# Kernel optimization log

Measured on AMD Instinct MI355X. Metric: run time of the kernel, lower is better.

The kernel has to match this reference:

```python
import jax, jax.numpy as jnp
import numpy as np

L = 32   # latent_dim == enc_dim
ND = 1   # node feature dim (single node type)
B, N = 8, 256
M = 3 * L           # message / Encoder output dim = 2*latent + enc = 96
DIN = 2 * (ND + L) + L  # Encoder input dim = 2*node + 2*latent + enc = 98


def _glorot(key, shape):
    fan_in, fan_out = shape
    s = jnp.sqrt(6.0 / (fan_in + fan_out))
    return jax.random.uniform(key, shape, jnp.float32, -s, s)


def setup_inputs() -> dict:
    key = jax.random.key(0)
    ks = jax.random.split(key, 14)
    return {
        "xs": jax.random.normal(ks[0], (B, N, ND), jnp.float32),
        "hs": jax.random.normal(ks[1], (B, N, L), jnp.float32),
        "e_feat": jax.random.normal(ks[2], (B, N, N, 1), jnp.float32),
        "adj": jax.random.randint(ks[3], (B, N, N), 0, 2, jnp.int32),
        "W_e": _glorot(ks[4], (1, L)),          # edge encoder
        "W_enc_lin": _glorot(ks[5], (DIN, M)),  # Encoder linear branch
        "W_enc_1": _glorot(ks[6], (DIN, M)),    # Encoder non-linear branch
        "W_enc_2": _glorot(ks[7], (M, M)),
        "W_proc_u": _glorot(ks[8], (M, L)),     # processor update
        "W_dec": _glorot(ks[9], (ND + 2 * L, ND)),
        "W_pred": _glorot(ks[10], (2 * L + L, 1)),
        "W_tm": _glorot(ks[11], (2 * L + L, L)),  # termination MPNN message
        "W_tu": _glorot(ks[12], (L, L)),          # termination MPNN update
        "W_term": _glorot(ks[13], (L, 1)),
    }


def reference(xs, hs, adj, e_feat, W_e, W_enc_lin, W_enc_1, W_enc_2,
              W_proc_u, W_dec, W_pred, W_tm, W_tu, W_term):
    b, n = adj.shape[0], adj.shape[1]
    adj2 = adj + jnp.eye(n, dtype=adj.dtype)[None]          # add self-loops
    mask = (adj2 > 0)[..., None]                            # [B,N,N,1]
    neg = jnp.float32(-jnp.inf)

    z = jnp.concatenate([xs, hs], axis=-1)                  # [B,N,ND+L]
    enc_e = jnp.einsum('bije,eh->bijh', e_feat, W_e)        # [B,N,N,L]

    zi = jnp.broadcast_to(z[:, :, None, :], (b, n, n, z.shape[-1]))
    zj = jnp.broadcast_to(z[:, None, :, :], (b, n, n, z.shape[-1]))
    u = jnp.concatenate([zi, zj, enc_e], axis=-1)           # [B,N,N,98]
    # Encoder: linear + 2-layer ReLU MLP (message function)
    msg = u @ W_enc_lin + jax.nn.relu(u @ W_enc_1) @ W_enc_2  # [B,N,N,96]
    agg = jnp.max(jnp.where(mask, msg, neg), axis=2)        # masked max over j
    new_h = agg @ W_proc_u                                  # [B,N,L]

    new_x = jnp.concatenate([z, new_h], axis=-1) @ W_dec    # decoder

    hi = jnp.broadcast_to(new_h[:, :, None, :], (b, n, n, L))
    hj = jnp.broadcast_to(new_h[:, None, :, :], (b, n, n, L))
    hij = jnp.concatenate([hi, hj, enc_e], axis=-1)         # [B,N,N,96]
    p = jnp.where(mask, hij @ W_pred, neg)                  # [B,N,N,1]

    # termination MPNN (tau_in == new_h for single node type)
    mt = jax.nn.relu(hij @ W_tm)                            # [B,N,N,L]
    tau_node = jnp.max(jnp.where(mask, mt, neg), axis=2) @ W_tu
    tau = jnp.mean(tau_node, axis=1) @ W_term               # [B,1]

    cat_h = new_h
    return new_x, p, tau, cat_h
```

## Files before the change

kernel.cpp:

```cpp
#include <hip/hip_runtime.h>
#include <hip/hip_bf16.h>
#include <math.h>

#define BB 8
#define NN 256
#define LLAT 32
#define MM 96
#define ZD 33
#define ROWS (BB*NN)

#define OFF_ALIN   0
#define OFF_BLIN   (OFF_ALIN + ROWS*MM)
#define OFF_A1     (OFF_BLIN + ROWS*MM)
#define OFF_B1     (OFF_A1   + ROWS*MM)
#define OFF_AGG    (OFF_B1   + ROWS*MM)
#define OFF_Z      (OFF_AGG  + ROWS*MM)
#define OFF_NEWH   (OFF_Z    + ROWS*ZD)
#define OFF_PI     (OFF_NEWH + ROWS*LLAT)
#define OFF_PJ     (OFF_PI   + ROWS)
#define OFF_TI     (OFF_PJ   + ROWS)
#define OFF_TJ     (OFF_TI   + ROWS*LLAT)
#define OFF_TAUM   (OFF_TJ   + ROWS*LLAT)
#define OFF_CONST  (OFF_TAUM + ROWS*LLAT)
#define C_LIN   0
#define C_1     96
#define C_PRED  192
#define C_TM    193
#define C_WCOMB 225
#define OFF_W2TH (OFF_CONST + 512)
#define OFF_W2TL (OFF_W2TH + 4992)

#define OUT_NEWX 0
#define OUT_P    2048
#define OUT_TAU  526336
#define OUT_CATH 526344

#define NEG_BIG (-3.0e38f)

typedef __attribute__((ext_vector_type(8))) short bf16x8;
typedef __attribute__((ext_vector_type(4))) float f32x4;

__device__ inline void bf16split(float v, ushort& hi, ushort& lo) {
  __hip_bfloat16 h = __float2bfloat16(v);
  float hf = __bfloat162float(h);
  __hip_bfloat16 l = __float2bfloat16(v - hf);
  hi = *reinterpret_cast<ushort*>(&h);
  lo = *reinterpret_cast<ushort*>(&l);
}

__global__ __launch_bounds__(256) void k_prep(
    const float* __restrict__ xs, const float* __restrict__ hs,
    const float* __restrict__ W_enc_lin, const float* __restrict__ W_enc_1,
    const float* __restrict__ W_e, const float* __restrict__ W_pred,
    const float* __restrict__ W_tm, const float* __restrict__ W_tu,
    const float* __restrict__ W_term, const float* __restrict__ W_enc_2,
    float* __restrict__ ws, float* __restrict__ out) {
  const int blk = blockIdx.x;
  const int t = threadIdx.x;

  if (blk < 256) {
    const int r0 = blk * 8;
    __shared__ float WzL[66 * 96];
    __shared__ float Wz1[66 * 96];
    __shared__ float zz[8][34];
    {
      const uint4* sL = (const uint4*)W_enc_lin;
      const uint4* s1 = (const uint4*)W_enc_1;
      uint4* dL = (uint4*)WzL;
      uint4* d1 = (uint4*)Wz1;
      for (int idx = t; idx < 1584; idx += 256) {
        dL[idx] = sL[idx];
        d1[idx] = s1[idx];
      }
    }
    {
      const int r = t >> 5, e = t & 31;
      zz[r][e + 1] = hs[(r0 + r) * 32 + e];
      if (t < 8) zz[t][0] = xs[r0 + t];
    }
    __syncthreads();
    for (int idx = t; idx < 8 * ZD; idx += 256) {
      const int r = idx / ZD, e = idx - r * ZD;
      ws[OFF_Z + (r0 + r) * ZD + e] = zz[r][e];
    }
    const int r = t >> 5;
    const int gr = r0 + r;
    #pragma unroll
    for (int q = 0; q < 3; ++q) {
      const int c = (t & 31) + 32 * q;
      float al = 0.f, bl = 0.f, a1 = 0.f, b1 = 0.f;
      #pragma unroll
      for (int k = 0; k < ZD; ++k) {
        const float zk = zz[r][k];
        al = fmaf(zk, WzL[k * 96 + c], al);
        bl = fmaf(zk, WzL[(ZD + k) * 96 + c], bl);
        a1 = fmaf(zk, Wz1[k * 96 + c], a1);
        b1 = fmaf(zk, Wz1[(ZD + k) * 96 + c], b1);
      }
      ws[OFF_ALIN + gr * 96 + c] = al;
      ws[OFF_BLIN + gr * 96 + c] = bl;
      ws[OFF_A1 + gr * 96 + c] = a1;
      ws[OFF_B1 + gr * 96 + c] = b1;
    }
  } else if (blk < 262) {
    const int c = (blk - 256) * 16 + (t >> 4);
    const int kk0 = (t & 15) * 6;
    ushort* w2h = (ushort*)(ws + OFF_W2TH);
    ushort* w2l = (ushort*)(ws + OFF_W2TL);
    #pragma unroll
    for (int q = 0; q < 6; ++q) {
      const int kk = kk0 + q;
      ushort hi, lo;
      bf16split(W_enc_2[kk * 96 + c], hi, lo);
      w2h[c * 104 + kk] = hi;
      w2l[c * 104 + kk] = lo;
    }
  } else if (blk == 262) {
    float* cst = ws + OFF_CONST;
    if (t < 96) {
      float s0 = 0.f, s1 = 0.f;
      for (int k = 0; k < 32; ++k) {
        float we = W_e[k];
        s0 = fmaf(we, W_enc_lin[(66 + k) * 96 + t], s0);
        s1 = fmaf(we, W_enc_1[(66 + k) * 96 + t], s1);
      }
      cst[C_LIN + t] = s0;
      cst[C_1 + t] = s1;
    }
  } else {
    float* cst = ws + OFF_CONST;
    if (t < 32) {
      float s_tm = 0.f;
      for (int k = 0; k < 32; ++k) s_tm = fmaf(W_e[k], W_tm[(64 + k) * 32 + t], s_tm);
      cst[C_TM + t] = s_tm;
      float s_wc = 0.f;
      for (int q = 0; q < 32; ++q) s_wc = fmaf(W_tu[t * 32 + q], W_term[q], s_wc);
      cst[C_WCOMB + t] = s_wc;
    } else if (t == 32) {
      float s = 0.f;
      for (int k = 0; k < 32; ++k) s = fmaf(W_e[k], W_pred[64 + k], s);
      cst[C_PRED] = s;
    } else if (t >= 40 && t < 48) {
      out[OUT_TAU + (t - 40)] = 0.f;
    }
  }
}

__global__ __launch_bounds__(512, 4) void k_main(
    const float* __restrict__ e_feat, const int* __restrict__ adj,
    const float* __restrict__ W_proc_u, const float* __restrict__ W_dec,
    const float* __restrict__ W_pred, const float* __restrict__ W_tm,
    float* __restrict__ ws, float* __restrict__ out) {
  const int bi = blockIdx.x;
  const int i = bi & 255;
  const int brow = bi & ~255;
  const int t = threadIdx.x;
  const int lane = t & 63, w = t >> 6;
  const int l15 = lane & 15, lg = lane >> 4;

  __shared__ __align__(16) ushort W2Ts[2 * 96 * 104];
  __shared__ float A1i[96], ALi[96], c1s[96], cls[96];
  __shared__ float red[8][96];
  __shared__ float aggs[96], nh[32];

  {
    const uint4* src = (const uint4*)(ws + OFF_W2TH);
    uint4* dst = (uint4*)W2Ts;
    for (int idx = t; idx < 2496; idx += 512) dst[idx] = src[idx];
  }
  if (t < 96) {
    A1i[t] = ws[OFF_A1 + bi * 96 + t];
    ALi[t] = ws[OFF_ALIN + bi * 96 + t];
    c1s[t] = ws[OFF_CONST + C_1 + t];
    cls[t] = ws[OFF_CONST + C_LIN + t];
  }

  const int jr0 = w * 32 + l15;
  const int jr1 = jr0 + 16;
  const float* b1base0 = ws + OFF_B1 + (brow + jr0) * 96 + lg * 8;
  const float* b1base1 = ws + OFF_B1 + (brow + jr1) * 96 + lg * 8;
  float4 b1r[2][3][2];
  #pragma unroll
  for (int ks = 0; ks < 3; ++ks) {
    b1r[0][ks][0] = ((const float4*)(b1base0 + ks * 32))[0];
    b1r[0][ks][1] = ((const float4*)(b1base0 + ks * 32))[1];
    b1r[1][ks][0] = ((const float4*)(b1base1 + ks * 32))[0];
    b1r[1][ks][1] = ((const float4*)(b1base1 + ks * 32))[1];
  }
  int adjv[2][4];
  float ejv[2][4];
  #pragma unroll
  for (int jg = 0; jg < 2; ++jg) {
    #pragma unroll
    for (int r = 0; r < 4; ++r) {
      const int j = w * 32 + jg * 16 + lg * 4 + r;
      adjv[jg][r] = adj[bi * 256 + j];
      ejv[jg][r] = e_feat[bi * 256 + j];
    }
  }
  const float ejA0 = e_feat[bi * 256 + jr0];
  const float ejA1 = e_feat[bi * 256 + jr1];

  __syncthreads();

  bf16x8 ah[2][3], al[2][3];
  #pragma unroll
  for (int ks = 0; ks < 3; ++ks) {
    const int ka = ks * 32 + lg * 8;
    float cc[8], aa[8];
    #pragma unroll
    for (int e = 0; e < 4; ++e) {
      cc[e] = c1s[ka + e];      cc[e + 4] = c1s[ka + 4 + e];
      aa[e] = A1i[ka + e];      aa[e + 4] = A1i[ka + 4 + e];
    }
    #pragma unroll
    for (int jg = 0; jg < 2; ++jg) {
      const float ej = jg ? ejA1 : ejA0;
      const float4 b0 = b1r[jg][ks][0], b1 = b1r[jg][ks][1];
      const float vvv[8] = {b0.x, b0.y, b0.z, b0.w, b1.x, b1.y, b1.z, b1.w};
      bf16x8 h8, l8;
      #pragma unroll
      for (int e = 0; e < 8; ++e) {
        float v = fmaxf(fmaf(ej, cc[e], aa[e] + vvv[e]), 0.f);
        ushort hi, lo;
        bf16split(v, hi, lo);
        h8[e] = (short)hi;
        l8[e] = (short)lo;
      }
      ah[jg][ks] = h8;
      al[jg][ks] = l8;
    }
  }

  f32x4 acc[2][6];
  #pragma unroll
  for (int jg = 0; jg < 2; ++jg)
    #pragma unroll
    for (int ct = 0; ct < 6; ++ct) acc[jg][ct] = 0;

  #pragma unroll
  for (int ks = 0; ks < 3; ++ks) {
    const int ka = ks * 32 + lg * 8;
    #pragma unroll
    for (int ct = 0; ct < 6; ++ct) {
      const int br = (ct * 16 + l15) * 104 + ka;
      const bf16x8 bh = *(const bf16x8*)&W2Ts[br];
      const bf16x8 bl = *(const bf16x8*)&W2Ts[96 * 104 + br];
      #pragma unroll
      for (int jg = 0; jg < 2; ++jg) {
        acc[jg][ct] = __builtin_amdgcn_mfma_f32_16x16x32_bf16(ah[jg][ks], bh, acc[jg][ct], 0, 0, 0);
        acc[jg][ct] = __builtin_amdgcn_mfma_f32_16x16x32_bf16(ah[jg][ks], bl, acc[jg][ct], 0, 0, 0);
        acc[jg][ct] = __builtin_amdgcn_mfma_f32_16x16x32_bf16(al[jg][ks], bh, acc[jg][ct], 0, 0, 0);
      }
    }
  }

  float aliC[6], clsC[6];
  #pragma unroll
  for (int ct = 0; ct < 6; ++ct) {
    const int c = ct * 16 + l15;
    aliC[ct] = ALi[c];
    clsC[ct] = cls[c];
  }
  float rmax[6] = {-INFINITY, -INFINITY, -INFINITY, -INFINITY, -INFINITY, -INFINITY};
  #pragma unroll
  for (int jg = 0; jg < 2; ++jg) {
    #pragma unroll
    for (int r = 0; r < 4; ++r) {
      const int j = w * 32 + jg * 16 + lg * 4 + r;
      const bool msk = (adjv[jg][r] > 0) || (j == i);
      if (msk) {
        const float ej = ejv[jg][r];
        const float* BL = ws + OFF_BLIN + (brow + j) * 96;
        #pragma unroll
        for (int ct = 0; ct < 6; ++ct) {
          float val = acc[jg][ct][r] + aliC[ct] + fmaf(clsC[ct], ej, BL[ct * 16 + l15]);
          rmax[ct] = fmaxf(rmax[ct], val);
        }
      }
    }
  }

  #pragma unroll
  for (int ct = 0; ct < 6; ++ct) {
    float v = rmax[ct];
    v = fmaxf(v, __shfl_xor(v, 16));
    v = fmaxf(v, __shfl_xor(v, 32));
    rmax[ct] = v;
  }
  if (lg == 0) {
    #pragma unroll
    for (int ct = 0; ct < 6; ++ct) red[w][ct * 16 + l15] = rmax[ct];
  }
  __syncthreads();
  if (t < 96) {
    float m = red[0][t];
    #pragma unroll
    for (int q = 1; q < 8; ++q) m = fmaxf(m, red[q][t]);
    aggs[t] = m;
  }
  __syncthreads();

  if (t < 32) {
    float s = 0.f;
    #pragma unroll 8
    for (int c = 0; c < 96; ++c) s = fmaf(aggs[c], W_proc_u[c * 32 + t], s);
    nh[t] = s;
    out[OUT_CATH + bi * 32 + t] = s;
  }
  __syncthreads();
  if (t < 32) {
    float si = 0.f, sj = 0.f;
    #pragma unroll
    for (int m = 0; m < 32; ++m) {
      si = fmaf(nh[m], W_tm[m * 32 + t], si);
      sj = fmaf(nh[m], W_tm[(32 + m) * 32 + t], sj);
    }
    ws[OFF_TI + bi * 32 + t] = si;
    ws[OFF_TJ + bi * 32 + t] = sj;
  } else if (t >= 64 && t < 128) {
    const int idx = t - 64;
    float v = 0.f;
    if (idx < ZD) v = ws[OFF_Z + bi * ZD + idx] * W_dec[idx];
    else if (idx < ZD + 32) v = nh[idx - ZD] * W_dec[idx];
    v += __shfl_xor(v, 1);
    v += __shfl_xor(v, 2);
    v += __shfl_xor(v, 4);
    v += __shfl_xor(v, 8);
    v += __shfl_xor(v, 16);
    v += __shfl_xor(v, 32);
    if (idx == 0) out[OUT_NEWX + bi] = v;
  } else if (t >= 128 && t < 192) {
    const int idx = t - 128;
    const int m = idx & 31;
    float v = nh[m] * W_pred[idx];
    v += __shfl_xor(v, 1);
    v += __shfl_xor(v, 2);
    v += __shfl_xor(v, 4);
    v += __shfl_xor(v, 8);
    v += __shfl_xor(v, 16);
    if (idx == 0) ws[OFF_PI + bi] = v;
    else if (idx == 32) ws[OFF_PJ + bi] = v;
  }
}

__global__ __launch_bounds__(256) void k_pair(
    const float* __restrict__ e_feat, const int* __restrict__ adj,
    float* __restrict__ ws, float* __restrict__ out) {
  const int bi = blockIdx.x;
  const int i = bi & 255;
  const int brow = bi & ~255;
  const int t = threadIdx.x;
  __shared__ float Tis[32], ctms[32], partial[8][32];
  __shared__ float ejr[256], pjr[256];
  __shared__ int mskr[256];
  __shared__ float Pis, cpred;

  ejr[t] = e_feat[bi * 256 + t];
  pjr[t] = ws[OFF_PJ + brow + t];
  mskr[t] = (adj[bi * 256 + t] > 0) || (t == i);
  if (t < 32) {
    Tis[t] = ws[OFF_TI + bi * 32 + t];
    ctms[t] = ws[OFF_CONST + C_TM + t];
  } else if (t == 32) {
    Pis = ws[OFF_PI + bi];
  } else if (t == 33) {
    cpred = ws[OFF_CONST + C_PRED];
  }
  __syncthreads();

  out[OUT_P + bi * 256 + t] =
      mskr[t] ? (Pis + pjr[t] + ejr[t] * cpred) : NEG_BIG;

  {
    const int k = t & 31, g = t >> 5;
    const float tik = Tis[k], ctk = ctms[k];
    const float* Tj = ws + OFF_TJ + brow * 32;
    float m = -INFINITY;
    #pragma unroll
    for (int jj = 0; jj < 32; ++jj) {
      const int j = g * 32 + jj;
      const float tjv = Tj[j * 32 + k];
      const float val = fmaxf(tik + fmaf(ejr[j], ctk, tjv), 0.f);
      m = mskr[j] ? fmaxf(m, val) : m;
    }
    partial[g][k] = m;
  }
  __syncthreads();
  if (t < 32) {
    float v = partial[0][t];
    #pragma unroll
    for (int g = 1; g < 8; ++g) v = fmaxf(v, partial[g][t]);
    float s = v * ws[OFF_CONST + C_WCOMB + t];
    s += __shfl_xor(s, 1);
    s += __shfl_xor(s, 2);
    s += __shfl_xor(s, 4);
    s += __shfl_xor(s, 8);
    s += __shfl_xor(s, 16);
    if (t == 0) atomicAdd(&out[OUT_TAU + (bi >> 8)], s * (1.0f / 256.0f));
  }
}

extern "C" void kernel_launch(void* const* d_in, const int* in_sizes, int n_in,
                              void* d_out, int out_size, void* d_ws, size_t ws_size,
                              hipStream_t stream) {
  const float* xs        = (const float*)d_in[0];
  const float* hs        = (const float*)d_in[1];
  const float* e_feat    = (const float*)d_in[2];
  const int*   adj       = (const int*)d_in[3];
  const float* W_e       = (const float*)d_in[4];
  const float* W_enc_lin = (const float*)d_in[5];
  const float* W_enc_1   = (const float*)d_in[6];
  const float* W_enc_2   = (const float*)d_in[7];
  const float* W_proc_u  = (const float*)d_in[8];
  const float* W_dec     = (const float*)d_in[9];
  const float* W_pred    = (const float*)d_in[10];
  const float* W_tm      = (const float*)d_in[11];
  const float* W_tu      = (const float*)d_in[12];
  const float* W_term    = (const float*)d_in[13];

  float* ws  = (float*)d_ws;
  float* out = (float*)d_out;

  k_prep<<<264, 256, 0, stream>>>(xs, hs, W_enc_lin, W_enc_1, W_e, W_pred,
                                  W_tm, W_tu, W_term, W_enc_2, ws, out);
  k_main<<<ROWS, 512, 0, stream>>>(e_feat, adj, W_proc_u, W_dec, W_pred, W_tm,
                                   ws, out);
  k_pair<<<ROWS, 256, 0, stream>>>(e_feat, adj, ws, out);
}
```

Before: 182.3 us.

## Process four rows i per k_main block to reuse staged W2 and B1 registers

k_main now handles IPB=4 consecutive rows i per block instead of one, looping over them. The bf16 W2 tile in shared memory and the per-thread B1 register fragments are loaded once and reused across the four rows, which amortises the staging cost. In exchange the grid shrinks to 512 blocks, the occupancy hint drops from 4 to 2, and each row iteration adds serialising barriers, so latency hiding and parallelism are reduced.

```diff
diff --git a/kernel.cpp b/kernel.cpp
--- a/kernel.cpp
+++ b/kernel.cpp
@@ -8,6 +8,7 @@
 #define MM 96
 #define ZD 33
 #define ROWS (BB*NN)
+#define IPB 4
 
 #define OFF_ALIN   0
 #define OFF_BLIN   (OFF_ALIN + ROWS*MM)
@@ -146,20 +147,22 @@
   }
 }
 
-__global__ __launch_bounds__(512, 4) void k_main(
+__global__ __launch_bounds__(512, 2) void k_main(
     const float* __restrict__ e_feat, const int* __restrict__ adj,
     const float* __restrict__ W_proc_u, const float* __restrict__ W_dec,
     const float* __restrict__ W_pred, const float* __restrict__ W_tm,
     float* __restrict__ ws, float* __restrict__ out) {
-  const int bi = blockIdx.x;
-  const int i = bi & 255;
-  const int brow = bi & ~255;
+  const int blk = blockIdx.x;
+  const int b = blk >> 6;
+  const int i0 = (blk & 63) * IPB;
+  const int brow = b * 256;
   const int t = threadIdx.x;
   const int lane = t & 63, w = t >> 6;
   const int l15 = lane & 15, lg = lane >> 4;
 
   __shared__ __align__(16) ushort W2Ts[2 * 96 * 104];
-  __shared__ float A1i[96], ALi[96], c1s[96], cls[96];
+  __shared__ float A1s[IPB][96], ALs[IPB][96];
+  __shared__ float c1s[96], cls[96];
   __shared__ float red[8][96];
   __shared__ float aggs[96], nh[32];
 
@@ -168,9 +171,12 @@
     uint4* dst = (uint4*)W2Ts;
     for (int idx = t; idx < 2496; idx += 512) dst[idx] = src[idx];
   }
+  for (int idx = t; idx < IPB * 96; idx += 512) {
+    const int r = idx / 96, c = idx - r * 96;
+    A1s[r][c] = ws[OFF_A1 + (brow + i0 + r) * 96 + c];
+    ALs[r][c] = ws[OFF_ALIN + (brow + i0 + r) * 96 + c];
+  }
   if (t < 96) {
-    A1i[t] = ws[OFF_A1 + bi * 96 + t];
-    ALi[t] = ws[OFF_ALIN + bi * 96 + t];
     c1s[t] = ws[OFF_CONST + C_1 + t];
     cls[t] = ws[OFF_CONST + C_LIN + t];
   }
@@ -187,160 +193,161 @@
     b1r[1][ks][0] = ((const float4*)(b1base1 + ks * 32))[0];
     b1r[1][ks][1] = ((const float4*)(b1base1 + ks * 32))[1];
   }
-  int adjv[2][4];
-  float ejv[2][4];
-  #pragma unroll
-  for (int jg = 0; jg < 2; ++jg) {
-    #pragma unroll
-    for (int r = 0; r < 4; ++r) {
-      const int j = w * 32 + jg * 16 + lg * 4 + r;
-      adjv[jg][r] = adj[bi * 256 + j];
-      ejv[jg][r] = e_feat[bi * 256 + j];
-    }
-  }
-  const float ejA0 = e_feat[bi * 256 + jr0];
-  const float ejA1 = e_feat[bi * 256 + jr1];
 
   __syncthreads();
 
-  bf16x8 ah[2][3], al[2][3];
-  #pragma unroll
-  for (int ks = 0; ks < 3; ++ks) {
-    const int ka = ks * 32 + lg * 8;
-    float cc[8], aa[8];
-    #pragma unroll
-    for (int e = 0; e < 4; ++e) {
-      cc[e] = c1s[ka + e];      cc[e + 4] = c1s[ka + 4 + e];
-      aa[e] = A1i[ka + e];      aa[e + 4] = A1i[ka + 4 + e];
-    }
+  for (int ii = 0; ii < IPB; ++ii) {
+    const int i = i0 + ii;
+    const int bi = brow + i;
+
+    const float ejA0 = e_feat[bi * 256 + jr0];
+    const float ejA1 = e_feat[bi * 256 + jr1];
+    int adjv[2][4];
+    float ejv[2][4];
     #pragma unroll
     for (int jg = 0; jg < 2; ++jg) {
-      const float ej = jg ? ejA1 : ejA0;
-      const float4 b0 = b1r[jg][ks][0], b1 = b1r[jg][ks][1];
-      const float vvv[8] = {b0.x, b0.y, b0.z, b0.w, b1.x, b1.y, b1.z, b1.w};
-      bf16x8 h8, l8;
-      #pragma unroll
-      for (int e = 0; e < 8; ++e) {
-        float v = fmaxf(fmaf(ej, cc[e], aa[e] + vvv[e]), 0.f);
-        ushort hi, lo;
-        bf16split(v, hi, lo);
-        h8[e] = (short)hi;
-        l8[e] = (short)lo;
-      }
-      ah[jg][ks] = h8;
-      al[jg][ks] = l8;
-    }
-  }
-
-  f32x4 acc[2][6];
-  #pragma unroll
-  for (int jg = 0; jg < 2; ++jg)
-    #pragma unroll
-    for (int ct = 0; ct < 6; ++ct) acc[jg][ct] = 0;
-
-  #pragma unroll
-  for (int ks = 0; ks < 3; ++ks) {
-    const int ka = ks * 32 + lg * 8;
+      #pragma unroll
+      for (int r = 0; r < 4; ++r) {
+        const int j = w * 32 + jg * 16 + lg * 4 + r;
+        adjv[jg][r] = adj[bi * 256 + j];
+        ejv[jg][r] = e_feat[bi * 256 + j];
+      }
+    }
+
+    bf16x8 ah[2][3], al[2][3];
+    #pragma unroll
+    for (int ks = 0; ks < 3; ++ks) {
+      const int ka = ks * 32 + lg * 8;
+      float cc[8], aa[8];
+      #pragma unroll
+      for (int e = 0; e < 4; ++e) {
+        cc[e] = c1s[ka + e];          cc[e + 4] = c1s[ka + 4 + e];
+        aa[e] = A1s[ii][ka + e];      aa[e + 4] = A1s[ii][ka + 4 + e];
+      }
+      #pragma unroll
+      for (int jg = 0; jg < 2; ++jg) {
+        const float ej = jg ? ejA1 : ejA0;
+        const float4 b0 = b1r[jg][ks][0], b1 = b1r[jg][ks][1];
+        const float vvv[8] = {b0.x, b0.y, b0.z, b0.w, b1.x, b1.y, b1.z, b1.w};
+        bf16x8 h8, l8;
+        #pragma unroll
+        for (int e = 0; e < 8; ++e) {
+          float v = fmaxf(fmaf(ej, cc[e], aa[e] + vvv[e]), 0.f);
+          ushort hi, lo;
+          bf16split(v, hi, lo);
+          h8[e] = (short)hi;
+          l8[e] = (short)lo;
+        }
+        ah[jg][ks] = h8;
+        al[jg][ks] = l8;
+      }
+    }
+
+    f32x4 acc[2][6];
+    #pragma unroll
+    for (int jg = 0; jg < 2; ++jg)
+      #pragma unroll
+      for (int ct = 0; ct < 6; ++ct) acc[jg][ct] = 0;
+
+    #pragma unroll
+    for (int ks = 0; ks < 3; ++ks) {
+      const int ka = ks * 32 + lg * 8;
+      #pragma unroll
+      for (int ct = 0; ct < 6; ++ct) {
+        const int br = (ct * 16 + l15) * 104 + ka;
+        const bf16x8 bh = *(const bf16x8*)&W2Ts[br];
+        const bf16x8 bl = *(const bf16x8*)&W2Ts[96 * 104 + br];
+        #pragma unroll
+        for (int jg = 0; jg < 2; ++jg) {
+          acc[jg][ct] = __builtin_amdgcn_mfma_f32_16x16x32_bf16(ah[jg][ks], bh, acc[jg][ct], 0, 0, 0);
+          acc[jg][ct] = __builtin_amdgcn_mfma_f32_16x16x32_bf16(ah[jg][ks], bl, acc[jg][ct], 0, 0, 0);
+          acc[jg][ct] = __builtin_amdgcn_mfma_f32_16x16x32_bf16(al[jg][ks], bh, acc[jg][ct], 0, 0, 0);
+        }
+      }
+    }
+
+    float rmax[6] = {-INFINITY, -INFINITY, -INFINITY, -INFINITY, -INFINITY, -INFINITY};
+    #pragma unroll
+    for (int jg = 0; jg < 2; ++jg) {
+      #pragma unroll
+      for (int r = 0; r < 4; ++r) {
+        const int j = w * 32 + jg * 16 + lg * 4 + r;
+        const bool msk = (adjv[jg][r] > 0) || (j == i);
+        if (msk) {
+          const float ej = ejv[jg][r];
+          const float* BL = ws + OFF_BLIN + (brow + j) * 96;
+          #pragma unroll
+          for (int ct = 0; ct < 6; ++ct) {
+            const int c = ct * 16 + l15;
+            float val = acc[jg][ct][r] + ALs[ii][c] + fmaf(cls[c], ej, BL[c]);
+            rmax[ct] = fmaxf(rmax[ct], val);
+          }
+        }
+      }
+    }
+
     #pragma unroll
     for (int ct = 0; ct < 6; ++ct) {
-      const int br = (ct * 16 + l15) * 104 + ka;
-      const bf16x8 bh = *(const bf16x8*)&W2Ts[br];
-      const bf16x8 bl = *(const bf16x8*)&W2Ts[96 * 104 + br];
-      #pragma unroll
-      for (int jg = 0; jg < 2; ++jg) {
-        acc[jg][ct] = __builtin_amdgcn_mfma_f32_16x16x32_bf16(ah[jg][ks], bh, acc[jg][ct], 0, 0, 0);
-        acc[jg][ct] = __builtin_amdgcn_mfma_f32_16x16x32_bf16(ah[jg][ks], bl, acc[jg][ct], 0, 0, 0);
-        acc[jg][ct] = __builtin_amdgcn_mfma_f32_16x16x32_bf16(al[jg][ks], bh, acc[jg][ct], 0, 0, 0);
-      }
-    }
-  }
-
-  float aliC[6], clsC[6];
-  #pragma unroll
-  for (int ct = 0; ct < 6; ++ct) {
-    const int c = ct * 16 + l15;
-    aliC[ct] = ALi[c];
-    clsC[ct] = cls[c];
-  }
-  float rmax[6] = {-INFINITY, -INFINITY, -INFINITY, -INFINITY, -INFINITY, -INFINITY};
-  #pragma unroll
-  for (int jg = 0; jg < 2; ++jg) {
-    #pragma unroll
-    for (int r = 0; r < 4; ++r) {
-      const int j = w * 32 + jg * 16 + lg * 4 + r;
-      const bool msk = (adjv[jg][r] > 0) || (j == i);
-      if (msk) {
-        const float ej = ejv[jg][r];
-        const float* BL = ws + OFF_BLIN + (brow + j) * 96;
-        #pragma unroll
-        for (int ct = 0; ct < 6; ++ct) {
-          float val = acc[jg][ct][r] + aliC[ct] + fmaf(clsC[ct], ej, BL[ct * 16 + l15]);
-          rmax[ct] = fmaxf(rmax[ct], val);
-        }
-      }
-    }
-  }
-
-  #pragma unroll
-  for (int ct = 0; ct < 6; ++ct) {
-    float v = rmax[ct];
-    v = fmaxf(v, __shfl_xor(v, 16));
-    v = fmaxf(v, __shfl_xor(v, 32));
-    rmax[ct] = v;
-  }
-  if (lg == 0) {
-    #pragma unroll
-    for (int ct = 0; ct < 6; ++ct) red[w][ct * 16 + l15] = rmax[ct];
-  }
-  __syncthreads();
-  if (t < 96) {
-    float m = red[0][t];
-    #pragma unroll
-    for (int q = 1; q < 8; ++q) m = fmaxf(m, red[q][t]);
-    aggs[t] = m;
-  }
-  __syncthreads();
-
-  if (t < 32) {
-    float s = 0.f;
-    #pragma unroll 8
-    for (int c = 0; c < 96; ++c) s = fmaf(aggs[c], W_proc_u[c * 32 + t], s);
-    nh[t] = s;
-    out[OUT_CATH + bi * 32 + t] = s;
-  }
-  __syncthreads();
-  if (t < 32) {
-    float si = 0.f, sj = 0.f;
-    #pragma unroll
-    for (int m = 0; m < 32; ++m) {
-      si = fmaf(nh[m], W_tm[m * 32 + t], si);
-      sj = fmaf(nh[m], W_tm[(32 + m) * 32 + t], sj);
-    }
-    ws[OFF_TI + bi * 32 + t] = si;
-    ws[OFF_TJ + bi * 32 + t] = sj;
-  } else if (t >= 64 && t < 128) {
-    const int idx = t - 64;
-    float v = 0.f;
-    if (idx < ZD) v = ws[OFF_Z + bi * ZD + idx] * W_dec[idx];
-    else if (idx < ZD + 32) v = nh[idx - ZD] * W_dec[idx];
-    v += __shfl_xor(v, 1);
-    v += __shfl_xor(v, 2);
-    v += __shfl_xor(v, 4);
-    v += __shfl_xor(v, 8);
-    v += __shfl_xor(v, 16);
-    v += __shfl_xor(v, 32);
-    if (idx == 0) out[OUT_NEWX + bi] = v;
-  } else if (t >= 128 && t < 192) {
-    const int idx = t - 128;
-    const int m = idx & 31;
-    float v = nh[m] * W_pred[idx];
-    v += __shfl_xor(v, 1);
-    v += __shfl_xor(v, 2);
-    v += __shfl_xor(v, 4);
-    v += __shfl_xor(v, 8);
-    v += __shfl_xor(v, 16);
-    if (idx == 0) ws[OFF_PI + bi] = v;
-    else if (idx == 32) ws[OFF_PJ + bi] = v;
+      float v = rmax[ct];
+      v = fmaxf(v, __shfl_xor(v, 16));
+      v = fmaxf(v, __shfl_xor(v, 32));
+      rmax[ct] = v;
+    }
+    if (lg == 0) {
+      #pragma unroll
+      for (int ct = 0; ct < 6; ++ct) red[w][ct * 16 + l15] = rmax[ct];
+    }
+    __syncthreads();
+    if (t < 96) {
+      float m = red[0][t];
+      #pragma unroll
+      for (int q = 1; q < 8; ++q) m = fmaxf(m, red[q][t]);
+      aggs[t] = m;
+    }
+    __syncthreads();
+
+    if (t < 32) {
+      float s = 0.f;
+      #pragma unroll 8
+      for (int c = 0; c < 96; ++c) s = fmaf(aggs[c], W_proc_u[c * 32 + t], s);
+      nh[t] = s;
+      out[OUT_CATH + bi * 32 + t] = s;
+    }
+    __syncthreads();
+    if (t < 32) {
+      float si = 0.f, sj = 0.f;
+      #pragma unroll
+      for (int m = 0; m < 32; ++m) {
+        si = fmaf(nh[m], W_tm[m * 32 + t], si);
+        sj = fmaf(nh[m], W_tm[(32 + m) * 32 + t], sj);
+      }
+      ws[OFF_TI + bi * 32 + t] = si;
+      ws[OFF_TJ + bi * 32 + t] = sj;
+    } else if (t >= 64 && t < 128) {
+      const int idx = t - 64;
+      float v = 0.f;
+      if (idx < ZD) v = ws[OFF_Z + bi * ZD + idx] * W_dec[idx];
+      else if (idx < ZD + 32) v = nh[idx - ZD] * W_dec[idx];
+      v += __shfl_xor(v, 1);
+      v += __shfl_xor(v, 2);
+      v += __shfl_xor(v, 4);
+      v += __shfl_xor(v, 8);
+      v += __shfl_xor(v, 16);
+      v += __shfl_xor(v, 32);
+      if (idx == 0) out[OUT_NEWX + bi] = v;
+    } else if (t >= 128 && t < 192) {
+      const int idx = t - 128;
+      const int m = idx & 31;
+      float v = nh[m] * W_pred[idx];
+      v += __shfl_xor(v, 1);
+      v += __shfl_xor(v, 2);
+      v += __shfl_xor(v, 4);
+      v += __shfl_xor(v, 8);
+      v += __shfl_xor(v, 16);
+      if (idx == 0) ws[OFF_PI + bi] = v;
+      else if (idx == 32) ws[OFF_PJ + bi] = v;
+    }
+    __syncthreads();
   }
 }
 
@@ -424,7 +431,7 @@
 
   k_prep<<<264, 256, 0, stream>>>(xs, hs, W_enc_lin, W_enc_1, W_e, W_pred,
                                   W_tm, W_tu, W_term, W_enc_2, ws, out);
-  k_main<<<ROWS, 512, 0, stream>>>(e_feat, adj, W_proc_u, W_dec, W_pred, W_tm,
-                                   ws, out);
+  k_main<<<ROWS / IPB, 512, 0, stream>>>(e_feat, adj, W_proc_u, W_dec, W_pred,
+                                         W_tm, ws, out);
   k_pair<<<ROWS, 256, 0, stream>>>(e_feat, adj, ws, out);
 }
```

Result: slower. 191.9 us (+5.3%).
